# Kernel tuning notes

Hardware: AMD Instinct MI355X
Metric: run time of the kernel (lower is better)

## Reference

```python
import jax, jax.numpy as jnp
import numpy as np

N_NODES = 50000
EMBED_DIM = 512
N_EDGES = 800000
NEG_SLOPE = 0.01  # nn.LeakyReLU default


def setup_inputs() -> dict:
    key = jax.random.key(0)
    k1, k2, k3 = jax.random.split(key, 3)
    X = jax.random.normal(k1, (N_NODES, EMBED_DIM), dtype=jnp.float32)
    # Glorot-ish scale for the GCNConv weight
    W = jax.random.normal(k2, (EMBED_DIM, EMBED_DIM), dtype=jnp.float32) / np.sqrt(EMBED_DIM)
    b = jnp.zeros((EMBED_DIM,), dtype=jnp.float32)
    edge_index = jax.random.randint(k3, (2, N_EDGES), 0, N_NODES, dtype=jnp.int32)
    return {"X": X, "W": W, "b": b, "edge_index": edge_index}


def reference(X, W, b, edge_index):
    N = X.shape[0]
    # GCNConv: add self-loops, symmetric normalization deg^-1/2 A deg^-1/2
    loop = jnp.arange(N, dtype=edge_index.dtype)
    src = jnp.concatenate([edge_index[0], loop])  # [E+N]
    dst = jnp.concatenate([edge_index[1], loop])  # [E+N]
    deg = jax.ops.segment_sum(jnp.ones_like(dst, dtype=X.dtype), dst, num_segments=N)
    dinv = jnp.where(deg > 0, jax.lax.rsqrt(deg), 0.0)  # deg^{-1/2}, inf->0
    norm = dinv[src] * dinv[dst]                         # [E+N]
    H = X @ W                                            # [N, D] dense GEMM
    msgs = H[src] * norm[:, None]                        # [E+N, D] gathered messages
    out = jax.ops.segment_sum(msgs, dst, num_segments=N) + b
    # LeakyReLU activation; Dropout is identity in eval mode
    return jnp.where(out >= 0, out, NEG_SLOPE * out)
```

## Files before the change

kernel.cpp:

```cpp
#include <hip/hip_runtime.h>
#include <cstdint>
#include <cstddef>

#define DFEAT 512
#define BM 128
#define BN 128
#define BK 32

typedef __attribute__((ext_vector_type(8))) short bf16x8;
typedef __attribute__((ext_vector_type(4))) float f32x4;

#define GLOBAL_AS __attribute__((address_space(1)))
#define LDS_AS __attribute__((address_space(3)))

__device__ __forceinline__ unsigned short f2bf(float f) {
  unsigned u = __float_as_uint(f);
  u = u + 0x7fffu + ((u >> 16) & 1u);
  return (unsigned short)(u >> 16);
}

__device__ __forceinline__ float bf2f_lo(unsigned u) { return __uint_as_float(u << 16); }
__device__ __forceinline__ float bf2f_hi(unsigned u) { return __uint_as_float(u & 0xffff0000u); }

__device__ __forceinline__ void gl_lds16(const void* g, void* l) {
  __builtin_amdgcn_global_load_lds((const GLOBAL_AS unsigned int*)g,
                                   (LDS_AS unsigned int*)l, 16, 0, 0);
}

__global__ void k_init(int* __restrict__ deg, int* __restrict__ fill, int N) {
  int i = blockIdx.x * blockDim.x + threadIdx.x;
  if (i < N) { deg[i] = 1; fill[i] = 0; }
}

__global__ void k_count(const int* __restrict__ dst, int* __restrict__ deg, int E) {
  int i = blockIdx.x * blockDim.x + threadIdx.x;
  if (i < E) atomicAdd(&deg[dst[i]], 1);
}

__global__ void k_dinv(const int* __restrict__ deg, float* __restrict__ dinv, int N) {
  int i = blockIdx.x * blockDim.x + threadIdx.x;
  if (i < N) dinv[i] = rsqrtf((float)deg[i]);
}

__global__ void k_scan(const int* __restrict__ deg, int* __restrict__ rowStart, int N) {
  const int t = threadIdx.x;
  const int C = (N + 1023) / 1024;
  int lo = t * C;
  int hi = lo + C; if (hi > N) hi = N; if (lo > N) lo = N;
  int sum = 0;
  for (int i = lo; i < hi; ++i) sum += deg[i];
  __shared__ int sm[1024];
  sm[t] = sum;
  __syncthreads();
  for (int d = 1; d < 1024; d <<= 1) {
    int v = (t >= d) ? sm[t - d] : 0;
    __syncthreads();
    sm[t] += v;
    __syncthreads();
  }
  int off = sm[t] - sum;
  for (int i = lo; i < hi; ++i) { rowStart[i] = off; off += deg[i]; }
  if (t == 1023) rowStart[N] = sm[1023];
}

__global__ void k_fill(const int* __restrict__ src, const int* __restrict__ dst,
                       const int* __restrict__ rowStart, int* __restrict__ fill,
                       int2* __restrict__ cw, const float* __restrict__ dinv, int E, int N) {
  int i = blockIdx.x * blockDim.x + threadIdx.x;
  if (i >= E + N) return;
  int d, s;
  if (i < E) { d = dst[i]; s = src[i]; }
  else       { d = i - E; s = d; }
  int pos = rowStart[d] + atomicAdd(&fill[d], 1);
  int2 q; q.x = s; q.y = __float_as_int(dinv[s]);
  cw[pos] = q;
}

__global__ void k_wt(const float* __restrict__ W, unsigned short* __restrict__ Wt) {
  int i = blockIdx.x * blockDim.x + threadIdx.x;
  int k = i >> 9, n = i & 511;
  Wt[(size_t)n * DFEAT + k] = f2bf(W[i]);
}

__global__ void k_xb(const float* __restrict__ X, unsigned short* __restrict__ Xb, int total8) {
  int i = blockIdx.x * blockDim.x + threadIdx.x;
  if (i >= total8) return;
  const float4 a = *reinterpret_cast<const float4*>(X + (size_t)i * 8);
  const float4 c = *reinterpret_cast<const float4*>(X + (size_t)i * 8 + 4);
  uint4 o;
  o.x = (unsigned)f2bf(a.x) | ((unsigned)f2bf(a.y) << 16);
  o.y = (unsigned)f2bf(a.z) | ((unsigned)f2bf(a.w) << 16);
  o.z = (unsigned)f2bf(c.x) | ((unsigned)f2bf(c.y) << 16);
  o.w = (unsigned)f2bf(c.z) | ((unsigned)f2bf(c.w) << 16);
  *reinterpret_cast<uint4*>(Xb + (size_t)i * 8) = o;
}

template <bool TAIL>
__device__ __forceinline__ void agg8(const unsigned short* __restrict__ Xb,
                                     const int2* __restrict__ cw,
                                     int p, int e, int lane, float* acc) {
  int2 q[8];
#pragma unroll
  for (int i = 0; i < 8; ++i) {
    int pi = p + i;
    if (TAIL) pi = (pi < e) ? pi : (e - 1);
    q[i] = cw[pi];
  }
  uint4 v[8];
#pragma unroll
  for (int i = 0; i < 8; ++i)
    v[i] = *reinterpret_cast<const uint4*>(Xb + (size_t)q[i].x * DFEAT + lane * 8);
#pragma unroll
  for (int i = 0; i < 8; ++i) {
    float w = __int_as_float(q[i].y);
    if (TAIL) w = (p + i < e) ? w : 0.0f;
    acc[0] = fmaf(w, bf2f_lo(v[i].x), acc[0]); acc[1] = fmaf(w, bf2f_hi(v[i].x), acc[1]);
    acc[2] = fmaf(w, bf2f_lo(v[i].y), acc[2]); acc[3] = fmaf(w, bf2f_hi(v[i].y), acc[3]);
    acc[4] = fmaf(w, bf2f_lo(v[i].z), acc[4]); acc[5] = fmaf(w, bf2f_hi(v[i].z), acc[5]);
    acc[6] = fmaf(w, bf2f_lo(v[i].w), acc[6]); acc[7] = fmaf(w, bf2f_hi(v[i].w), acc[7]);
  }
}

__global__ __launch_bounds__(256) void k_aggregate(const unsigned short* __restrict__ Xb,
                                                   const int2* __restrict__ cw,
                                                   const int* __restrict__ rowStart,
                                                   const float* __restrict__ dinv,
                                                   unsigned short* __restrict__ Y, int N) {
  const int row = blockIdx.x * 4 + (threadIdx.x >> 6);
  const int lane = threadIdx.x & 63;
  float acc[8] = {0.f, 0.f, 0.f, 0.f, 0.f, 0.f, 0.f, 0.f};
  if (row < N) {
    const int s = rowStart[row], e = rowStart[row + 1];
    int p = s;
    for (; p + 8 <= e; p += 8) agg8<false>(Xb, cw, p, e, lane, acc);
    if (p < e) agg8<true>(Xb, cw, p, e, lane, acc);
    const float sc = dinv[row];
#pragma unroll
    for (int j = 0; j < 8; ++j) acc[j] *= sc;
  }
  uint4 o;
  o.x = (unsigned)f2bf(acc[0]) | ((unsigned)f2bf(acc[1]) << 16);
  o.y = (unsigned)f2bf(acc[2]) | ((unsigned)f2bf(acc[3]) << 16);
  o.z = (unsigned)f2bf(acc[4]) | ((unsigned)f2bf(acc[5]) << 16);
  o.w = (unsigned)f2bf(acc[6]) | ((unsigned)f2bf(acc[7]) << 16);
  *reinterpret_cast<uint4*>(Y + (size_t)row * DFEAT + lane * 8) = o;
}

__global__ __launch_bounds__(256) void k_gemm(const unsigned short* __restrict__ Y,
                                              const unsigned short* __restrict__ Wt,
                                              const float* __restrict__ bias,
                                              float* __restrict__ out, int M) {
  __shared__ unsigned short As[BM * BK];
  __shared__ unsigned short Bs[BN * BK];
  const int tid = threadIdx.x;
  const int lane = tid & 63;
  const int wave = tid >> 6;
  const int l16 = lane & 15;
  const int quad = lane >> 4;
  const int wm = (wave >> 1) * 64;
  const int wn = (wave & 1) * 64;

  const int nwg = gridDim.x;
  const int q8 = nwg >> 3, r8 = nwg & 7;
  const int xcd = blockIdx.x & 7, loc = blockIdx.x >> 3;
  const int wg = (xcd < r8 ? xcd * (q8 + 1) : r8 * (q8 + 1) + (xcd - r8) * q8) + loc;
  const int m0 = (wg >> 2) * BM;
  const int n0 = (wg & 3) * BN;

  f32x4 acc[4][4];
#pragma unroll
  for (int mi = 0; mi < 4; ++mi)
#pragma unroll
    for (int ni = 0; ni < 4; ++ni) { f32x4 z = {0.f, 0.f, 0.f, 0.f}; acc[mi][ni] = z; }

  const int ci0 = wave * 64 + lane;
  const int ci1 = 256 + ci0;
  const int ra0 = ci0 >> 2, ka0 = (((ci0 & 3) - (ra0 >> 1)) & 3) * 8;
  const int ra1 = ci1 >> 2, ka1 = (((ci1 & 3) - (ra1 >> 1)) & 3) * 8;

  const unsigned short* Ag0 = Y + (size_t)(m0 + ra0) * DFEAT + ka0;
  const unsigned short* Ag1 = Y + (size_t)(m0 + ra1) * DFEAT + ka1;
  const unsigned short* Bg0 = Wt + (size_t)(n0 + ra0) * DFEAT + ka0;
  const unsigned short* Bg1 = Wt + (size_t)(n0 + ra1) * DFEAT + ka1;
  unsigned short* La0 = As + ci0 * 8;
  unsigned short* La1 = As + ci1 * 8;
  unsigned short* Lb0 = Bs + ci0 * 8;
  unsigned short* Lb1 = Bs + ci1 * 8;

  const int rotA = (quad + ((wm + l16) >> 1)) & 3;
  const int rotB = (quad + ((wn + l16) >> 1)) & 3;
  const unsigned short* AsRd = As + (wm + l16) * BK + rotA * 8;
  const unsigned short* BsRd = Bs + (wn + l16) * BK + rotB * 8;

  for (int kk = 0; kk < DFEAT; kk += BK) {
    gl_lds16(Ag0 + kk, La0);
    gl_lds16(Ag1 + kk, La1);
    gl_lds16(Bg0 + kk, Lb0);
    gl_lds16(Bg1 + kk, Lb1);
    __syncthreads();
    bf16x8 av[4], bv[4];
#pragma unroll
    for (int mi = 0; mi < 4; ++mi)
      av[mi] = *reinterpret_cast<const bf16x8*>(AsRd + mi * 16 * BK);
#pragma unroll
    for (int ni = 0; ni < 4; ++ni)
      bv[ni] = *reinterpret_cast<const bf16x8*>(BsRd + ni * 16 * BK);
#pragma unroll
    for (int mi = 0; mi < 4; ++mi)
#pragma unroll
      for (int ni = 0; ni < 4; ++ni)
        acc[mi][ni] = __builtin_amdgcn_mfma_f32_16x16x32_bf16(av[mi], bv[ni], acc[mi][ni], 0, 0, 0);
    __syncthreads();
  }

  float bvals[4];
#pragma unroll
  for (int ni = 0; ni < 4; ++ni) bvals[ni] = bias[n0 + wn + 16 * ni + l16];

#pragma unroll
  for (int mi = 0; mi < 4; ++mi) {
#pragma unroll
    for (int r = 0; r < 4; ++r) {
      int row = m0 + wm + 16 * mi + quad * 4 + r;
      if (row < M) {
#pragma unroll
        for (int ni = 0; ni < 4; ++ni) {
          float v = acc[mi][ni][r] + bvals[ni];
          v = (v >= 0.f) ? v : 0.01f * v;
          out[(size_t)row * DFEAT + n0 + wn + 16 * ni + l16] = v;
        }
      }
    }
  }
}

extern "C" void kernel_launch(void* const* d_in, const int* in_sizes, int n_in,
                              void* d_out, int out_size, void* d_ws, size_t ws_size,
                              hipStream_t stream) {
  const float* X = (const float*)d_in[0];
  const float* W = (const float*)d_in[1];
  const float* b = (const float*)d_in[2];
  const int* ei  = (const int*)d_in[3];
  const int D = DFEAT;
  const int N = in_sizes[0] / D;
  const int E = in_sizes[3] / 2;
  const int* src = ei;
  const int* dst = ei + E;
  float* out = (float*)d_out;

  uintptr_t p = (uintptr_t)d_ws;
  auto carve = [&](size_t bytes) -> void* {
    uintptr_t r = p;
    p += (bytes + 255) & ~(size_t)255;
    return (void*)r;
  };
  int*   deg      = (int*)carve(sizeof(int) * (size_t)N);
  int*   fill     = (int*)carve(sizeof(int) * (size_t)N);
  int*   rowStart = (int*)carve(sizeof(int) * (size_t)(N + 1));
  float* dinv     = (float*)carve(sizeof(float) * (size_t)N);
  int2*  cw       = (int2*)carve(sizeof(int2) * (size_t)(E + N));
  unsigned short* Wt = (unsigned short*)carve(sizeof(unsigned short) * (size_t)D * D);
  const int Mtiles = (N + BM - 1) / BM;
  const int Mpad = Mtiles * BM;
  unsigned short* Y  = (unsigned short*)carve(sizeof(unsigned short) * (size_t)Mpad * D);

  unsigned short* Xb = (unsigned short*)d_out;

  hipLaunchKernelGGL(k_init,  dim3((N + 255) / 256), dim3(256), 0, stream, deg, fill, N);
  hipLaunchKernelGGL(k_count, dim3((E + 255) / 256), dim3(256), 0, stream, dst, deg, E);
  hipLaunchKernelGGL(k_dinv,  dim3((N + 255) / 256), dim3(256), 0, stream, deg, dinv, N);
  hipLaunchKernelGGL(k_scan,  dim3(1), dim3(1024), 0, stream, deg, rowStart, N);
  hipLaunchKernelGGL(k_fill,  dim3((E + N + 255) / 256), dim3(256), 0, stream,
                     src, dst, rowStart, fill, cw, dinv, E, N);
  hipLaunchKernelGGL(k_wt,    dim3((D * D) / 256), dim3(256), 0, stream, W, Wt);
  hipLaunchKernelGGL(k_xb,    dim3((N * D / 8 + 255) / 256), dim3(256), 0, stream,
                     X, Xb, N * D / 8);
  hipLaunchKernelGGL(k_aggregate, dim3(Mpad / 4), dim3(256), 0, stream,
                     Xb, cw, rowStart, dinv, Y, N);
  hipLaunchKernelGGL(k_gemm,  dim3(Mtiles * 4), dim3(256), 0, stream, Y, Wt, b, out, N);
}
```

Before: 501.4 us.

## Streamline CSR build: coalesced chunked scan, drop dinv kernel, fuse conversions

Replaces the single-block strided scan with a chunked, int4-vectorized scan that also writes per-row fill cursors. This removes the separate fill array and its zero-init, and lets k_fill use a single atomic per edge. The dinv kernel is dropped and rsqrt is recomputed inline from deg, and the W-transpose and X-to-bf16 kernels are merged into one launch. The aggregate kernel is split into two half launches, which adds a launch without an obvious benefit.

Measured after the change: 454.7 us. 1.1x faster.

```diff
diff --git a/kernel.cpp b/kernel.cpp
--- a/kernel.cpp
+++ b/kernel.cpp
@@ -27,9 +27,9 @@
                                    (LDS_AS unsigned int*)l, 16, 0, 0);
 }
 
-__global__ void k_init(int* __restrict__ deg, int* __restrict__ fill, int N) {
+__global__ void k_init(int* __restrict__ deg, int N) {
   int i = blockIdx.x * blockDim.x + threadIdx.x;
-  if (i < N) { deg[i] = 1; fill[i] = 0; }
+  if (i < N) deg[i] = 1;
 }
 
 __global__ void k_count(const int* __restrict__ dst, int* __restrict__ deg, int E) {
@@ -37,53 +37,75 @@
   if (i < E) atomicAdd(&deg[dst[i]], 1);
 }
 
-__global__ void k_dinv(const int* __restrict__ deg, float* __restrict__ dinv, int N) {
-  int i = blockIdx.x * blockDim.x + threadIdx.x;
-  if (i < N) dinv[i] = rsqrtf((float)deg[i]);
-}
-
-__global__ void k_scan(const int* __restrict__ deg, int* __restrict__ rowStart, int N) {
+__global__ __launch_bounds__(1024) void k_scan(const int* __restrict__ deg,
+                                               int* __restrict__ rowStart,
+                                               int* __restrict__ fillPos, int N) {
   const int t = threadIdx.x;
-  const int C = (N + 1023) / 1024;
-  int lo = t * C;
-  int hi = lo + C; if (hi > N) hi = N; if (lo > N) lo = N;
-  int sum = 0;
-  for (int i = lo; i < hi; ++i) sum += deg[i];
   __shared__ int sm[1024];
-  sm[t] = sum;
+  __shared__ int carrySm;
+  if (t == 0) carrySm = 0;
+  for (int base = 0; base < N; base += 4096) {
+    const int idx = base + t * 4;
+    int4 v = make_int4(0, 0, 0, 0);
+    if (idx + 3 < N) {
+      v = *reinterpret_cast<const int4*>(deg + idx);
+    } else if (idx < N) {
+      v.x = deg[idx];
+      if (idx + 1 < N) v.y = deg[idx + 1];
+      if (idx + 2 < N) v.z = deg[idx + 2];
+    }
+    const int s4 = v.x + v.y + v.z + v.w;
+    __syncthreads();
+    sm[t] = s4;
+    __syncthreads();
+    for (int d = 1; d < 1024; d <<= 1) {
+      const int o = (t >= d) ? sm[t - d] : 0;
+      __syncthreads();
+      sm[t] += o;
+      __syncthreads();
+    }
+    const int incl = sm[t];
+    const int carry = carrySm;
+    __syncthreads();
+    if (t == 1023) carrySm = carry + incl;
+    const int e0 = carry + incl - s4;
+    if (idx + 3 < N) {
+      int4 o4 = make_int4(e0, e0 + v.x, e0 + v.x + v.y, e0 + v.x + v.y + v.z);
+      *reinterpret_cast<int4*>(rowStart + idx) = o4;
+      *reinterpret_cast<int4*>(fillPos + idx) = o4;
+    } else if (idx < N) {
+      rowStart[idx] = e0; fillPos[idx] = e0;
+      if (idx + 1 < N) { rowStart[idx + 1] = e0 + v.x; fillPos[idx + 1] = e0 + v.x; }
+      if (idx + 2 < N) { rowStart[idx + 2] = e0 + v.x + v.y; fillPos[idx + 2] = e0 + v.x + v.y; }
+    }
+  }
   __syncthreads();
-  for (int d = 1; d < 1024; d <<= 1) {
-    int v = (t >= d) ? sm[t - d] : 0;
-    __syncthreads();
-    sm[t] += v;
-    __syncthreads();
-  }
-  int off = sm[t] - sum;
-  for (int i = lo; i < hi; ++i) { rowStart[i] = off; off += deg[i]; }
-  if (t == 1023) rowStart[N] = sm[1023];
+  if (t == 0) rowStart[N] = carrySm;
 }
 
 __global__ void k_fill(const int* __restrict__ src, const int* __restrict__ dst,
-                       const int* __restrict__ rowStart, int* __restrict__ fill,
-                       int2* __restrict__ cw, const float* __restrict__ dinv, int E, int N) {
+                       int* __restrict__ fillPos, int2* __restrict__ cw,
+                       const int* __restrict__ deg, int E, int N) {
   int i = blockIdx.x * blockDim.x + threadIdx.x;
   if (i >= E + N) return;
   int d, s;
   if (i < E) { d = dst[i]; s = src[i]; }
   else       { d = i - E; s = d; }
-  int pos = rowStart[d] + atomicAdd(&fill[d], 1);
-  int2 q; q.x = s; q.y = __float_as_int(dinv[s]);
+  int pos = atomicAdd(&fillPos[d], 1);
+  int2 q; q.x = s; q.y = __float_as_int(rsqrtf((float)deg[s]));
   cw[pos] = q;
 }
 
-__global__ void k_wt(const float* __restrict__ W, unsigned short* __restrict__ Wt) {
-  int i = blockIdx.x * blockDim.x + threadIdx.x;
-  int k = i >> 9, n = i & 511;
-  Wt[(size_t)n * DFEAT + k] = f2bf(W[i]);
-}
-
-__global__ void k_xb(const float* __restrict__ X, unsigned short* __restrict__ Xb, int total8) {
-  int i = blockIdx.x * blockDim.x + threadIdx.x;
+__global__ void k_wtxb(const float* __restrict__ W, unsigned short* __restrict__ Wt,
+                       const float* __restrict__ X, unsigned short* __restrict__ Xb,
+                       int total8) {
+  if (blockIdx.x < 1024) {
+    int i = blockIdx.x * 256 + threadIdx.x;
+    int k = i >> 9, n = i & 511;
+    Wt[(size_t)n * DFEAT + k] = f2bf(W[i]);
+    return;
+  }
+  int i = (blockIdx.x - 1024) * 256 + threadIdx.x;
   if (i >= total8) return;
   const float4 a = *reinterpret_cast<const float4*>(X + (size_t)i * 8);
   const float4 c = *reinterpret_cast<const float4*>(X + (size_t)i * 8 + 4);
@@ -124,9 +146,10 @@
 __global__ __launch_bounds__(256) void k_aggregate(const unsigned short* __restrict__ Xb,
                                                    const int2* __restrict__ cw,
                                                    const int* __restrict__ rowStart,
-                                                   const float* __restrict__ dinv,
-                                                   unsigned short* __restrict__ Y, int N) {
-  const int row = blockIdx.x * 4 + (threadIdx.x >> 6);
+                                                   const int* __restrict__ deg,
+                                                   unsigned short* __restrict__ Y,
+                                                   int N, int rowOff) {
+  const int row = rowOff + blockIdx.x * 4 + (threadIdx.x >> 6);
   const int lane = threadIdx.x & 63;
   float acc[8] = {0.f, 0.f, 0.f, 0.f, 0.f, 0.f, 0.f, 0.f};
   if (row < N) {
@@ -134,7 +157,7 @@
     int p = s;
     for (; p + 8 <= e; p += 8) agg8<false>(Xb, cw, p, e, lane, acc);
     if (p < e) agg8<true>(Xb, cw, p, e, lane, acc);
-    const float sc = dinv[row];
+    const float sc = rsqrtf((float)deg[row]);
 #pragma unroll
     for (int j = 0; j < 8; ++j) acc[j] *= sc;
   }
@@ -255,9 +278,8 @@
     return (void*)r;
   };
   int*   deg      = (int*)carve(sizeof(int) * (size_t)N);
-  int*   fill     = (int*)carve(sizeof(int) * (size_t)N);
   int*   rowStart = (int*)carve(sizeof(int) * (size_t)(N + 1));
-  float* dinv     = (float*)carve(sizeof(float) * (size_t)N);
+  int*   fillPos  = (int*)carve(sizeof(int) * (size_t)N);
   int2*  cw       = (int2*)carve(sizeof(int2) * (size_t)(E + N));
   unsigned short* Wt = (unsigned short*)carve(sizeof(unsigned short) * (size_t)D * D);
   const int Mtiles = (N + BM - 1) / BM;
@@ -266,16 +288,19 @@
 
   unsigned short* Xb = (unsigned short*)d_out;
 
-  hipLaunchKernelGGL(k_init,  dim3((N + 255) / 256), dim3(256), 0, stream, deg, fill, N);
+  const int total8 = N * D / 8;
+  const int half = (Mpad / 2 + 3) & ~3;
+
+  hipLaunchKernelGGL(k_init,  dim3((N + 255) / 256), dim3(256), 0, stream, deg, N);
   hipLaunchKernelGGL(k_count, dim3((E + 255) / 256), dim3(256), 0, stream, dst, deg, E);
-  hipLaunchKernelGGL(k_dinv,  dim3((N + 255) / 256), dim3(256), 0, stream, deg, dinv, N);
-  hipLaunchKernelGGL(k_scan,  dim3(1), dim3(1024), 0, stream, deg, rowStart, N);
+  hipLaunchKernelGGL(k_scan,  dim3(1), dim3(1024), 0, stream, deg, rowStart, fillPos, N);
   hipLaunchKernelGGL(k_fill,  dim3((E + N + 255) / 256), dim3(256), 0, stream,
-                     src, dst, rowStart, fill, cw, dinv, E, N);
-  hipLaunchKernelGGL(k_wt,    dim3((D * D) / 256), dim3(256), 0, stream, W, Wt);
-  hipLaunchKernelGGL(k_xb,    dim3((N * D / 8 + 255) / 256), dim3(256), 0, stream,
-                     X, Xb, N * D / 8);
-  hipLaunchKernelGGL(k_aggregate, dim3(Mpad / 4), dim3(256), 0, stream,
-                     Xb, cw, rowStart, dinv, Y, N);
+                     src, dst, fillPos, cw, deg, E, N);
+  hipLaunchKernelGGL(k_wtxb,  dim3(1024 + (total8 + 255) / 256), dim3(256), 0, stream,
+                     W, Wt, X, Xb, total8);
+  hipLaunchKernelGGL(k_aggregate, dim3(half / 4), dim3(256), 0, stream,
+                     Xb, cw, rowStart, deg, Y, N, 0);
+  hipLaunchKernelGGL(k_aggregate, dim3((Mpad - half) / 4), dim3(256), 0, stream,
+                     Xb, cw, rowStart, deg, Y, N, half);
   hipLaunchKernelGGL(k_gemm,  dim3(Mtiles * 4), dim3(256), 0, stream, Y, Wt, b, out, N);
 }
```
